# Optimization experiments

Hardware: AMD Instinct MI355X
Metric: run time of the kernel (lower is better)

## Reference

```python
import jax, jax.numpy as jnp
import numpy as np

B, T, V, E, H, M, U, W = 8, 64, 30000, 256, 512, 512, 32, 512


def setup_inputs():
    rng = np.random.RandomState(0)
    ks = jax.random.split(jax.random.key(0), 20)
    u_len = rng.randint(U // 2, U + 1, size=B).astype(np.int32)
    w_len = rng.randint(W // 2, W + 1, size=B).astype(np.int32)
    # word2utt[b, j] = utterance index owning word j; padded words -> last valid utt
    w2u = np.zeros((B, W), np.int32)
    for b in range(B):
        j = np.minimum(np.arange(W), w_len[b] - 1)
        w2u[b] = np.minimum((j * u_len[b]) // w_len[b], u_len[b] - 1)
    s = 0.02
    p = lambda i, shp: jax.random.normal(ks[i], shp, jnp.float32) * s
    emb = p(0, (V, E)).at[0].set(0.0)  # padding_idx=0
    return {
        'target': jax.random.randint(ks[1], (B, T), 0, V, jnp.int32),
        'u_output': jax.random.normal(ks[2], (B, U, M), jnp.float32),
        'w_output': jax.random.normal(ks[3], (B, W, M), jnp.float32),
        'u_len': jnp.asarray(u_len), 'w_len': jnp.asarray(w_len), 'word2utt': jnp.asarray(w2u),
        'emb': emb,
        'W_ih': p(4, (3 * H, E)), 'W_hh': p(5, (3 * H, H)),
        'b_ih': p(6, (3 * H,)), 'b_hh': p(7, (3 * H,)),
        'Wu': p(8, (H, M)), 'bu': p(9, (H,)),
        'Ww': p(10, (H, M)), 'bw': p(11, (H,)),
        'Wo': p(12, (V, H + M)), 'bo': p(13, (V,)),
        'Wd': p(14, (1, V)), 'Wy': p(15, (1, E)),
        'Ws': p(16, (1, H)), 'bs': p(17, (1,)),
    }


def reference(target, u_output, w_output, u_len, w_len, word2utt,
              emb, W_ih, W_hh, b_ih, b_hh, Wu, bu, Ww, bw, Wo, bo, Wd, Wy, Ws, bs):
    Bn = target.shape[0]
    Un = u_output.shape[1]
    Vn = Wo.shape[0]
    Au = jnp.einsum('bum,hm->buh', u_output, Wu) + bu  # attention_u(u_output)
    Aw = jnp.einsum('bwm,hm->bwh', w_output, Ww) + bw  # attention_w(w_output)
    u_mask = jnp.arange(Un)[None, :] < u_len[:, None]               # [B,U]
    w_mask = jnp.arange(w_output.shape[1])[None, :] < w_len[:, None]  # [B,W]
    # initial hidden = last valid utterance state (mem_hidden == dec_hidden)
    h0 = jnp.take_along_axis(u_output, (u_len - 1)[:, None, None], axis=1)[:, 0, :]

    def gru_step(x, h):
        gi = x @ W_ih.T + b_ih
        gh = h @ W_hh.T + b_hh
        ir, iz, inn = jnp.split(gi, 3, axis=-1)
        hr, hz, hn = jnp.split(gh, 3, axis=-1)
        r = jax.nn.sigmoid(ir + hr)
        z = jax.nn.sigmoid(iz + hz)
        n = jnp.tanh(inn + r * hn)
        return (1.0 - z) * n + z * h

    def seg_softmax(sw, seg, valid):  # per-batch ragged per-utterance softmax over words
        swm = jnp.where(valid, sw, -jnp.inf)
        m = jax.ops.segment_max(swm, seg, num_segments=Un)
        e = jnp.where(valid, jnp.exp(sw - m[seg]), 0.0)
        d = jax.ops.segment_sum(e, seg, num_segments=Un)
        return e / d[seg]

    def step(carry, yt):
        h, d_prev, eu_prev = carry
        y = emb[yt]                               # [B,E]
        h_new = gru_step(y, h)                    # rnn_output == new hidden (1 layer)
        su = jnp.einsum('bh,buh->bu', h_new, Au)
        su = jax.nn.softmax(jnp.where(u_mask, su, -jnp.inf), axis=-1)
        gamma = jax.nn.sigmoid(d_prev @ Wd.T + y @ Wy.T + h_new @ Ws.T + bs)  # [B,1]
        su = (1.0 - gamma) * su + gamma * eu_prev
        su = su / jnp.sum(su, axis=-1, keepdims=True)
        sw = jnp.einsum('bh,bwh->bw', h_new, Aw)
        pw = jax.vmap(seg_softmax)(sw, word2utt, w_mask)        # [B,W]
        suw = jnp.take_along_axis(su, word2utt, axis=1) * pw    # [B,W]
        ctx = jnp.einsum('bw,bwm->bm', suw, w_output)
        logits = jnp.concatenate([ctx, h_new], axis=-1) @ Wo.T + bo
        dt = jax.nn.log_softmax(logits, axis=-1)
        return (h_new, dt, su), (dt, suw, su)

    init = (h0, jnp.zeros((Bn, Vn), jnp.float32), jnp.zeros((Bn, Un), jnp.float32))
    _, (dts, suws, sus) = jax.lax.scan(step, init, target.T)
    dec_output = jnp.swapaxes(dts, 0, 1)   # [B,T,V]
    scores_uw = jnp.swapaxes(suws, 0, 1)   # [B,T,W]
    scores_u = jnp.swapaxes(sus, 0, 1)     # [B,T,U]
    return dec_output, scores_uw, scores_u
```

## Files before the change

### kernel.cpp

```cpp
#include <hip/hip_runtime.h>
#include <math.h>

typedef unsigned short ushort_t;
typedef unsigned int uint_t;
typedef unsigned long long ulong_t;
typedef __attribute__((ext_vector_type(8))) short s16x8;
typedef __attribute__((ext_vector_type(4))) float f32x4;

#define BB 8
#define TT 64
#define VV 30000
#define VP 30080
#define EE 256
#define HH 512
#define MM 512
#define UU 32
#define WW 512
#define G3 1536
#define NDB 235
#define NBG 64

#define OFF_GI    0
#define OFF_YALL  786432
#define OFF_WY    917504
#define OFF_H0    918016
#define OFF_HALL  922112
#define OFF_HU    1184256
#define OFF_HW    1446400
#define OFF_HS    1708544
#define OFF_HWV   1709056
#define OFF_P     1709568
#define OFF_SW    1725952
#define OFF_C     1988096
#define OFF_E     6182400
#define OFF_WV    6198784
#define OFF_PART  6200320
#define OFF_LSE   6208512
#define OFF_WOV   6209024
#define OFF_HBT   13909504
#define OFF_SYNC  14040576

#define DEC_SZ (BB*TT*VV)
#define SUW_OFF DEC_SZ
#define SU_OFF  (DEC_SZ + BB*TT*WW)

__device__ __forceinline__ float sigm(float x){ return 1.0f/(1.0f+__expf(-x)); }
__device__ __forceinline__ ushort_t to_bf16(float f){
  uint_t u = __float_as_uint(f);
  return (ushort_t)((u + 0x7fffu + ((u>>16)&1u)) >> 16);
}


template<int TRANSB>
__global__ void __launch_bounds__(256)
k_gemm_b(const float* __restrict__ A, int lda, int aS,
         const float* __restrict__ B, int ldb, int bS,
         const float* __restrict__ bias,
         float* __restrict__ C, int ldc, int cS, int K){
  A += (size_t)blockIdx.z * aS;
  B += (size_t)blockIdx.z * bS;
  C += (size_t)blockIdx.z * cS;
  __shared__ float As[32][65];
  __shared__ float Bs[32][65];
  int tid = threadIdx.x;
  int bx = blockIdx.x, by = blockIdx.y;
  int tx = tid & 15, ty = tid >> 4;
  float acc[4][4] = {};
  for (int k0 = 0; k0 < K; k0 += 32){
    {
      int r = tid >> 2, cbase = (tid & 3) * 8;
      const float* ap = A + (size_t)(by*64 + r)*lda + k0 + cbase;
      #pragma unroll
      for (int i=0;i<8;++i) As[cbase+i][r] = ap[i];
    }
    if (TRANSB){
      int r = tid >> 2, cbase = (tid & 3) * 8;
      const float* bp = B + (size_t)(bx*64 + r)*ldb + k0 + cbase;
      #pragma unroll
      for (int i=0;i<8;++i) Bs[cbase+i][r] = bp[i];
    } else {
      int kk = tid >> 3, cbase = (tid & 7) * 8;
      const float* bp = B + (size_t)(k0 + kk)*ldb + bx*64 + cbase;
      #pragma unroll
      for (int i=0;i<8;++i) Bs[kk][cbase+i] = bp[i];
    }
    __syncthreads();
    #pragma unroll
    for (int kk=0;kk<32;++kk){
      float a0=As[kk][ty*4+0], a1=As[kk][ty*4+1], a2=As[kk][ty*4+2], a3=As[kk][ty*4+3];
      float b0=Bs[kk][tx*4+0], b1=Bs[kk][tx*4+1], b2=Bs[kk][tx*4+2], b3=Bs[kk][tx*4+3];
      acc[0][0]+=a0*b0; acc[0][1]+=a0*b1; acc[0][2]+=a0*b2; acc[0][3]+=a0*b3;
      acc[1][0]+=a1*b0; acc[1][1]+=a1*b1; acc[1][2]+=a1*b2; acc[1][3]+=a1*b3;
      acc[2][0]+=a2*b0; acc[2][1]+=a2*b1; acc[2][2]+=a2*b2; acc[2][3]+=a2*b3;
      acc[3][0]+=a3*b0; acc[3][1]+=a3*b1; acc[3][2]+=a3*b2; acc[3][3]+=a3*b3;
    }
    __syncthreads();
  }
  #pragma unroll
  for (int i=0;i<4;++i){
    int row = by*64 + ty*4 + i;
    #pragma unroll
    for (int j=0;j<4;++j){
      int col = bx*64 + tx*4 + j;
      float v = acc[i][j];
      if (bias) v += bias[col];
      C[(size_t)row*ldc + col] = v;
    }
  }
}

__global__ void k_gather_y(const int* __restrict__ target, const float* __restrict__ emb,
                           float* __restrict__ ws){
  int idx = blockIdx.x*256 + threadIdx.x;
  int bt = idx >> 8; int e = idx & 255;
  int tok = target[bt];
  ws[OFF_YALL + idx] = emb[tok*EE + e];
}

__global__ void k_wy(const float* __restrict__ Wy, float* __restrict__ ws){
  int wid  = blockIdx.x*4 + (threadIdx.x>>6);
  int lane = threadIdx.x & 63;
  const float* y = ws + OFF_YALL + wid*EE;
  float acc = 0.f;
  for (int e=lane; e<EE; e+=64) acc += y[e]*Wy[e];
  for (int off=32; off; off>>=1) acc += __shfl_xor(acc, off);
  if (lane == 0) ws[OFF_WY + wid] = acc;
}

__global__ void k_h0(const float* __restrict__ u_output, const int* __restrict__ u_len,
                     float* __restrict__ ws){
  int idx = blockIdx.x*256 + threadIdx.x;
  int b = idx >> 9; int k = idx & 511;
  int u = u_len[b]-1;
  ws[OFF_H0 + idx] = u_output[(b*UU+u)*MM + k];
}

__global__ void __launch_bounds__(256)
k_wovc(const float* __restrict__ Wo, ushort_t* __restrict__ wov){
  int idx8 = blockIdx.x*256 + threadIdx.x;
  int v = idx8 >> 6;
  int k8 = (idx8 & 63) << 3;
  uint_t u0=0,u1=0,u2=0,u3=0;
  if (v < VV){
    const float* src = Wo + (size_t)v*1024 + k8;
    float4 f0 = *(const float4*)src;
    float4 f1 = *(const float4*)(src+4);
    u0 = (uint_t)to_bf16(f0.x) | ((uint_t)to_bf16(f0.y) << 16);
    u1 = (uint_t)to_bf16(f0.z) | ((uint_t)to_bf16(f0.w) << 16);
    u2 = (uint_t)to_bf16(f1.x) | ((uint_t)to_bf16(f1.y) << 16);
    u3 = (uint_t)to_bf16(f1.z) | ((uint_t)to_bf16(f1.w) << 16);
  }
  uint4 pk = make_uint4(u0,u1,u2,u3);
  *(uint4*)(wov + (size_t)idx8*8) = pk;
}

__global__ void __launch_bounds__(256)
k_wv(const float* __restrict__ Wo, const float* __restrict__ bo,
     const float* __restrict__ Wd, float* __restrict__ wv){
  __shared__ float wds[128];
  __shared__ float red[256];
  int tid = threadIdx.x;
  int v0 = blockIdx.x*128;
  float pbo=0.f, pwd=0.f;
  if (tid < 128){
    int v = v0 + tid;
    float wd = (v<VV)? Wd[v] : 0.f;
    wds[tid] = wd;
    pbo = wd * ((v<VV)? bo[v] : 0.f);
    pwd = wd;
  }
  __syncthreads();
  float4 acc = {0,0,0,0};
  int nmax = (v0 + 128 <= VV) ? 128 : (VV - v0);
  for (int i=0;i<nmax;++i){
    float wd = wds[i];
    float4 w4 = *(const float4*)(Wo + (size_t)(v0+i)*1024 + tid*4);
    acc.x += wd*w4.x; acc.y += wd*w4.y; acc.z += wd*w4.z; acc.w += wd*w4.w;
  }
  atomicAdd(&wv[tid*4+0], acc.x);
  atomicAdd(&wv[tid*4+1], acc.y);
  atomicAdd(&wv[tid*4+2], acc.z);
  atomicAdd(&wv[tid*4+3], acc.w);
  red[tid] = pbo; __syncthreads();
  for (int s=128; s; s>>=1){ if (tid<s) red[tid]+=red[tid+s]; __syncthreads(); }
  if (tid==0) atomicAdd(&wv[1024], red[0]);
  __syncthreads();
  red[tid] = pwd; __syncthreads();
  for (int s=128; s; s>>=1){ if (tid<s) red[tid]+=red[tid+s]; __syncthreads(); }
  if (tid==0) atomicAdd(&wv[1025], red[0]);
}


__global__ void __launch_bounds__(512)
k_gru_persist(const float* __restrict__ W_hh, const float* __restrict__ b_hh,
              float* __restrict__ ws){
  uint_t* flags = (uint_t*)(ws + OFF_SYNC);
  int k    = blockIdx.x*8 + (threadIdx.x>>6);
  int lane = threadIdx.x & 63;
  const float* gi_all = ws + OFF_GI;
  const float* wr = W_hh + (size_t)k*HH;
  const float* wz = W_hh + (size_t)(HH+k)*HH;
  const float* wn = W_hh + (size_t)(2*HH+k)*HH;
  float bhr = b_hh[k], bhz = b_hh[HH+k], bhn = b_hh[2*HH+k];

  for (int t=0; t<TT; ++t){
    const float* hin = (t==0) ? (ws+OFF_H0) : (ws+OFF_HALL + (size_t)(t-1)*4096);
    float* hout = ws + OFF_HALL + (size_t)t*4096;
    float pr[8], pz[8], pn[8];
    #pragma unroll
    for (int b=0;b<8;++b){ pr[b]=0.f; pz[b]=0.f; pn[b]=0.f; }
    #pragma unroll 2
    for (int kk=lane; kk<HH; kk+=64){
      float w1 = wr[kk], w2 = wz[kk], w3 = wn[kk];
      #pragma unroll
      for (int b=0;b<8;++b){
        float hv = hin[b*HH+kk];
        pr[b] += hv*w1; pz[b] += hv*w2; pn[b] += hv*w3;
      }
    }
    #pragma unroll
    for (int off=32; off; off>>=1){
      #pragma unroll
      for (int b=0;b<8;++b){
        pr[b] += __shfl_xor(pr[b],off);
        pz[b] += __shfl_xor(pz[b],off);
        pn[b] += __shfl_xor(pn[b],off);
      }
    }
    if (lane == 0){
      #pragma unroll
      for (int b=0;b<8;++b){
        const float* gi = gi_all + (b*TT + t)*G3;
        float r = sigm(gi[k]      + pr[b] + bhr);
        float z = sigm(gi[HH+k]   + pz[b] + bhz);
        float n = tanhf(gi[2*HH+k] + r*(pn[b] + bhn));
        hout[b*HH+k] = (1.f-z)*n + z*hin[b*HH+k];
      }
    }
    __syncthreads();
    if (threadIdx.x == 0)
      __hip_atomic_store(&flags[blockIdx.x*32], (uint_t)(t+1), __ATOMIC_RELEASE, __HIP_MEMORY_SCOPE_AGENT);
    if ((int)threadIdx.x < NBG){
      while (__hip_atomic_load(&flags[threadIdx.x*32], __ATOMIC_RELAXED, __HIP_MEMORY_SCOPE_AGENT) < (uint_t)(t+1))
        __builtin_amdgcn_s_sleep(1);
    }
    __syncthreads();
  }
  {
    ushort_t* hbt = (ushort_t*)(ws + OFF_HBT);
    int base = (blockIdx.x*512 + threadIdx.x)*8;
    #pragma unroll
    for (int i=0;i<8;++i) hbt[base+i] = to_bf16(ws[OFF_HALL + base + i]);
  }
}


__global__ void __launch_bounds__(256)
k_lh_mfma(const float* __restrict__ Wo, const float* __restrict__ bo,
          const ushort_t* __restrict__ hbt, float* __restrict__ out){
  int tid = threadIdx.x;
  int wv = tid >> 6, l = tid & 63;
  int lm = l & 15, lg = l >> 4;
  int vbase = blockIdx.x*128 + wv*32;
  int rbase = blockIdx.y*128;
  f32x4 acc[2][8];
  #pragma unroll
  for (int s=0;s<2;++s)
    #pragma unroll
    for (int rt=0;rt<8;++rt) acc[s][rt] = (f32x4){0.f,0.f,0.f,0.f};

  for (int k0 = 0; k0 < 512; k0 += 32){
    int kk = k0 + lg*8;
    union { uint_t u[4]; s16x8 s; } af[2];
    #pragma unroll
    for (int s=0;s<2;++s){
      int v = vbase + s*16 + lm; if (v >= VV) v = VV-1;
      const float* ap = Wo + (size_t)v*1024 + 512 + kk;
      float4 f0 = *(const float4*)ap;
      float4 f1 = *(const float4*)(ap+4);
      af[s].u[0] = ((__float_as_uint(f0.x)+0x8000u)>>16) | ((__float_as_uint(f0.y)+0x8000u) & 0xffff0000u);
      af[s].u[1] = ((__float_as_uint(f0.z)+0x8000u)>>16) | ((__float_as_uint(f0.w)+0x8000u) & 0xffff0000u);
      af[s].u[2] = ((__float_as_uint(f1.x)+0x8000u)>>16) | ((__float_as_uint(f1.y)+0x8000u) & 0xffff0000u);
      af[s].u[3] = ((__float_as_uint(f1.z)+0x8000u)>>16) | ((__float_as_uint(f1.w)+0x8000u) & 0xffff0000u);
    }
    #pragma unroll
    for (int rt=0;rt<8;++rt){
      const ushort_t* bp = hbt + (size_t)(rbase + rt*16 + lm)*HH + kk;
      s16x8 bf = *(const s16x8*)bp;
      acc[0][rt] = __builtin_amdgcn_mfma_f32_16x16x32_bf16(af[0].s, bf, acc[0][rt], 0, 0, 0);
      acc[1][rt] = __builtin_amdgcn_mfma_f32_16x16x32_bf16(af[1].s, bf, acc[1][rt], 0, 0, 0);
    }
  }
  float bv[2][4];
  #pragma unroll
  for (int s=0;s<2;++s)
    #pragma unroll
    for (int r=0;r<4;++r){
      int v = vbase + s*16 + lg*4 + r;
      bv[s][r] = (v < VV) ? bo[v] : 0.f;
    }
  #pragma unroll
  for (int rt=0;rt<8;++rt){
    int row = rbase + rt*16 + lm;
    float* orow = out + (size_t)((row&7)*TT + (row>>3))*VV;
    #pragma unroll
    for (int s=0;s<2;++s){
      #pragma unroll
      for (int r=0;r<4;++r){
        int v = vbase + s*16 + lg*4 + r;
        if (v < VV) orow[v] = acc[s][rt][r] + bv[s][r];
      }
    }
  }
}


__global__ void k_hdots(const float* __restrict__ Ws, float* __restrict__ ws){
  int wid  = blockIdx.x*4 + (threadIdx.x>>6);
  int lane = threadIdx.x & 63;
  int row = wid >> 1, which = wid & 1;
  const float* h = ws + OFF_HALL + row*HH;
  const float* src = which ? (ws + OFF_WV + 512) : Ws;
  float acc = 0.f;
  for (int k=lane; k<HH; k+=64) acc += h[k]*src[k];
  for (int off=32; off; off>>=1) acc += __shfl_xor(acc, off);
  if (lane == 0) (which ? ws+OFF_HWV : ws+OFF_HS)[row] = acc;
}

__global__ void k_p(const float* __restrict__ u_output, const int* __restrict__ u_len,
                    float* __restrict__ ws){
  int row = blockIdx.x;
  int b = row & 7;
  int tid = threadIdx.x;
  __shared__ float su_s[UU];
  {
    int u = tid >> 3, l8 = tid & 7;
    const float* hu = ws + OFF_HU + row*512;
    const float* uo = u_output + (size_t)(b*UU + u)*MM;
    float acc = 0.f;
    for (int m=l8; m<MM; m+=8) acc += hu[m]*uo[m];
    acc += __shfl_xor(acc,1); acc += __shfl_xor(acc,2); acc += __shfl_xor(acc,4);
    if (l8 == 0) su_s[u] = acc;
  }
  __syncthreads();
  if (tid < 32){
    int ul = u_len[b];
    float sv = su_s[tid];
    bool valid = tid < ul;
    float mv = valid ? sv : -1e30f;
    for (int off=16; off; off>>=1) mv = fmaxf(mv, __shfl_xor(mv, off));
    float e = valid ? __expf(sv - mv) : 0.f;
    float ssum = e;
    for (int off=16; off; off>>=1) ssum += __shfl_xor(ssum, off);
    ws[OFF_P + row*UU + tid] = e/ssum;
  }
}

__global__ void k_pw(const int* __restrict__ word2utt, const int* __restrict__ w_len,
                     float* __restrict__ ws){
  int row = blockIdx.x;
  int b = row & 7;
  int tid = threadIdx.x;
  __shared__ float sarr[WW];
  __shared__ int   seg[WW];
  __shared__ float marr[UU], darr[UU];
  int wl = w_len[b];
  float* swrow = ws + OFF_SW + row*WW;
  for (int w=tid; w<WW; w+=256){ sarr[w] = swrow[w]; seg[w] = word2utt[b*WW+w]; }
  __syncthreads();
  {
    int g = tid>>3, l8 = tid&7;
    float mv = -1e30f;
    for (int w=l8; w<wl; w+=8) if (seg[w]==g) mv = fmaxf(mv, sarr[w]);
    mv = fmaxf(mv, __shfl_xor(mv,1)); mv = fmaxf(mv, __shfl_xor(mv,2)); mv = fmaxf(mv, __shfl_xor(mv,4));
    float d = 0.f;
    for (int w=l8; w<wl; w+=8) if (seg[w]==g) d += __expf(sarr[w]-mv);
    d += __shfl_xor(d,1); d += __shfl_xor(d,2); d += __shfl_xor(d,4);
    if (l8 == 0){ marr[g]=mv; darr[g]=d; }
  }
  __syncthreads();
  for (int w=tid; w<WW; w+=256){
    float val = 0.f;
    if (w < wl){ int u = seg[w]; val = __expf(sarr[w]-marr[u])/darr[u]; }
    swrow[w] = val;
  }
}

__global__ void __launch_bounds__(256)
k_C(const float* __restrict__ w_output, const int* __restrict__ w_len,
    const int* __restrict__ u_len, const int* __restrict__ word2utt,
    float* __restrict__ ws){
  int row = blockIdx.x;
  int b = row & 7;
  int tid = threadIdx.x;
  __shared__ float pws[WW];
  __shared__ int   seg[WW];
  __shared__ int   st[UU], en[UU];
  __shared__ float wvs[512];
  __shared__ float red4[8];
  int wl = w_len[b], ul = u_len[b];
  const float* pwrow = ws + OFF_SW + row*WW;
  for (int w=tid; w<WW; w+=256){ pws[w] = pwrow[w]; seg[w] = word2utt[b*WW+w]; }
  for (int m=tid; m<512; m+=256) wvs[m] = ws[OFF_WV + m];
  if (tid < UU){ st[tid]=0; en[tid]=0; }
  __syncthreads();
  for (int w=tid; w<wl; w+=256){
    int s = seg[w];
    if (w==0 || seg[w-1]!=s) st[s]=w;
    if (w==wl-1 || seg[w+1]!=s) en[s]=w+1;
  }
  __syncthreads();
  ushort_t* Cu = (ushort_t*)(ws + OFF_C);
  int m0 = tid, m1 = tid + 256;
  int lane = tid & 63, wvi = tid >> 6;
  for (int u=0; u<UU; ++u){
    float acc0=0.f, acc1=0.f;
    if (u < ul){
      int s = st[u], e = en[u];
      for (int w=s; w<e; ++w){
        float p = pws[w];
        const float* wo = w_output + ((size_t)(b*WW+w))*MM;
        acc0 += p*wo[m0];
        acc1 += p*wo[m1];
      }
    }
    size_t cbase = ((size_t)row*UU + u)*512;
    Cu[cbase + m0] = to_bf16(acc0);
    Cu[cbase + m1] = to_bf16(acc1);
    float part = acc0*wvs[m0] + acc1*wvs[m1];
    for (int off=32; off; off>>=1) part += __shfl_xor(part, off);
    if (lane == 0) red4[wvi] = part;
    __syncthreads();
    if (tid == 0) ws[OFF_E + row*UU + u] = red4[0]+red4[1]+red4[2]+red4[3];
    __syncthreads();
  }
}


__global__ void __launch_bounds__(256)
k_decode_persist(const int* __restrict__ u_len, const float* __restrict__ bs,
                 const ushort_t* __restrict__ wov,
                 float* __restrict__ ws, float* __restrict__ out){
  int bid = blockIdx.x;
  int tid = threadIdx.x;
  uint_t* sy     = (uint_t*)(ws + OFF_SYNC);
  uint_t* flags  = sy + 8192;
  uint_t* flags2 = sy + 16000;
  __shared__ float suL[8][32];
  __shared__ float qbufL[8], lseL[8], gamL[8];
  __shared__ int   ulS[8];
  __shared__ uint_t cbU[16*260];
  __shared__ float2 wred[4][8];
  __shared__ float smr[256], ssr[256];
  __shared__ float cst[4];
  if (tid == 0){ cst[0]=bs[0]; cst[1]=ws[OFF_WV+1024]; cst[2]=ws[OFF_WV+1025]; }
  if (tid < 8){ qbufL[tid]=0.f; lseL[tid]=0.f; ulS[tid]=u_len[tid]; }
  suL[tid>>5][tid&31] = 0.f;
  for (int i=tid; i<8*260; i+=256) cbU[8*260 + i] = 0u;
  __syncthreads();

  int wv = tid >> 6, l = tid & 63;
  int lm = l & 15, lgp = l >> 4;

  for (int t=0; t<TT; ++t){
    int b = tid >> 5, j = tid & 31;
    int row = t*8 + b;

    if (t > 0 && tid < 8)
      lseL[tid] = __hip_atomic_load((const float*)(ws + OFF_LSE + (t-1)*8 + tid),
                                    __ATOMIC_RELAXED, __HIP_MEMORY_SCOPE_AGENT);
    __syncthreads();
    if (tid < 8){
      float pd = 0.f;
      if (t > 0)
        pd = qbufL[tid] + ws[OFF_HWV + (t-1)*8 + tid] + cst[1] - lseL[tid]*cst[2];
      gamL[tid] = sigm(pd + ws[OFF_WY + tid*TT + t] + ws[OFF_HS + t*8 + tid] + cst[0]);
    }
    __syncthreads();
    {
      float gg = gamL[b];
      float p = ws[OFF_P + row*UU + j];
      float eu = suL[b][j];
      float mix = (1.f-gg)*p + gg*eu;
      float s2 = mix;
      #pragma unroll
      for (int off=16; off; off>>=1) s2 += __shfl_xor(s2, off);
      float su = mix / s2;
      suL[b][j] = su;
      float qp = su * ws[OFF_E + row*UU + j];
      #pragma unroll
      for (int off=16; off; off>>=1) qp += __shfl_xor(qp, off);
      if (j == 0) qbufL[b] = qp;
    }
    __syncthreads();
    if (bid < 8 && tid < 32)
      out[SU_OFF + (bid*TT + t)*UU + tid] = suL[bid][tid];
    {
      int m16 = j * 16;
      int ul = ulS[b];
      const ushort_t* Crow = (const ushort_t*)(ws + OFF_C) + ((size_t)row*UU)*512 + m16;
      float acc[16];
      #pragma unroll
      for (int i=0;i<16;++i) acc[i]=0.f;
      for (int u=0; u<ul; ++u){
        float su = suL[b][u];
        uint4 c0 = *(const uint4*)(Crow + (size_t)u*512);
        uint4 c1 = *(const uint4*)(Crow + (size_t)u*512 + 8);
        uint_t cc[8] = {c0.x,c0.y,c0.z,c0.w,c1.x,c1.y,c1.z,c1.w};
        #pragma unroll
        for (int q=0;q<8;++q){
          acc[2*q]   += su * __uint_as_float((cc[q] & 0xffffu) << 16);
          acc[2*q+1] += su * __uint_as_float((cc[q] >> 16) << 16);
        }
      }
      #pragma unroll
      for (int q=0;q<8;++q){
        uint_t pk = (uint_t)to_bf16(acc[2*q]) | ((uint_t)to_bf16(acc[2*q+1]) << 16);
        cbU[b*260 + j*8 + q] = pk;
      }
    }
    __syncthreads();

    {
      int v0w = bid*128 + wv*32;
      f32x4 acc0 = {0.f,0.f,0.f,0.f}, acc1 = {0.f,0.f,0.f,0.f};
      const ushort_t* ap0 = wov + (size_t)(v0w + lm)*512 + lgp*8;
      const ushort_t* ap1 = ap0 + 16*512;
      const uint_t* cbrow = cbU + lm*260 + lgp*4;
      #pragma unroll
      for (int ks=0; ks<16; ++ks){
        s16x8 av0 = *(const s16x8*)(ap0 + ks*32);
        s16x8 av1 = *(const s16x8*)(ap1 + ks*32);
        s16x8 bv  = *(const s16x8*)(cbrow + ks*16);
        acc0 = __builtin_amdgcn_mfma_f32_16x16x32_bf16(av0, bv, acc0, 0, 0, 0);
        acc1 = __builtin_amdgcn_mfma_f32_16x16x32_bf16(av1, bv, acc1, 0, 0, 0);
      }
      float pm = -1e30f, ps = 0.f;
      if (lm < 8){
        float* orow = out + ((size_t)(lm*TT + t))*VV;
        float l8v[8];
        #pragma unroll
        for (int vt=0; vt<2; ++vt){
          int vb = v0w + vt*16 + lgp*4;
          f32x4 a = vt ? acc1 : acc0;
          if (vb + 3 < VV){
            float4 o = *(const float4*)(orow + vb);
            float g0 = a[0]+o.x, g1 = a[1]+o.y, g2 = a[2]+o.z, g3 = a[3]+o.w;
            *(float4*)(orow + vb) = make_float4(g0,g1,g2,g3);
            l8v[vt*4+0]=g0; l8v[vt*4+1]=g1; l8v[vt*4+2]=g2; l8v[vt*4+3]=g3;
          } else {
            #pragma unroll
            for (int r=0;r<4;++r){
              int v = vb + r;
              float g = -1e30f;
              if (v < VV){ g = a[r] + orow[v]; orow[v] = g; }
              l8v[vt*4+r] = g;
            }
          }
        }
        #pragma unroll
        for (int i=0;i<8;++i) pm = fmaxf(pm, l8v[i]);
        #pragma unroll
        for (int i=0;i<8;++i) ps += (l8v[i] > -5e29f) ? __expf(l8v[i]-pm) : 0.f;
      }
      #pragma unroll
      for (int off=16; off<=32; off<<=1){
        float mo = __shfl_xor(pm, off);
        float so = __shfl_xor(ps, off);
        float nm = fmaxf(pm, mo);
        ps = ps*__expf(pm-nm) + so*__expf(mo-nm);
        pm = nm;
      }
      if (lgp == 0 && lm < 8) wred[wv][lm] = make_float2(pm, ps);
    }
    __syncthreads();
    if (tid < 8){
      float m = -1e30f, s = 0.f;
      #pragma unroll
      for (int w=0; w<4; ++w){
        float2 e = wred[w][tid];
        float nm = fmaxf(m, e.x);
        s = s*__expf(m-nm) + e.y*__expf(e.x-nm);
        m = nm;
      }
      *(float2*)(ws + OFF_PART + (t&1)*4096 + (bid*8 + tid)*2) = make_float2(m, s);
    }

    __syncthreads();
    if (tid == 0)
      __hip_atomic_store(&flags[bid*32], (uint_t)(t+1), __ATOMIC_RELEASE, __HIP_MEMORY_SCOPE_AGENT);
    if (bid < 8){
      if (tid < NDB){
        while (__hip_atomic_load(&flags[tid*32], __ATOMIC_RELAXED, __HIP_MEMORY_SCOPE_AGENT) < (uint_t)(t+1))
          __builtin_amdgcn_s_sleep(2);
      }
      __syncthreads();
      {
        const ulong_t* partq = (const ulong_t*)(ws + OFF_PART + (t&1)*4096);
        float m = -1e30f, s = 0.f;
        if (tid < NDB){
          ulong_t pq = __hip_atomic_load(&partq[tid*8 + bid], __ATOMIC_RELAXED, __HIP_MEMORY_SCOPE_AGENT);
          m = __uint_as_float((uint_t)pq);
          s = __uint_as_float((uint_t)(pq >> 32));
        }
        smr[tid]=m; ssr[tid]=s; __syncthreads();
        for (int st=128; st; st>>=1){
          if (tid < st){
            float m1 = smr[tid], s1 = ssr[tid];
            float m2 = smr[tid+st], s2 = ssr[tid+st];
            float mm = fmaxf(m1, m2);
            ssr[tid] = s1*__expf(m1-mm) + s2*__expf(m2-mm);
            smr[tid] = mm;
          }
          __syncthreads();
        }
        if (tid == 0){
          __hip_atomic_store((float*)(ws + OFF_LSE + t*8 + bid), smr[0] + logf(ssr[0]),
                             __ATOMIC_RELAXED, __HIP_MEMORY_SCOPE_AGENT);
          __hip_atomic_store(&flags2[bid*32], (uint_t)(t+1), __ATOMIC_RELEASE, __HIP_MEMORY_SCOPE_AGENT);
        }
      }
    }
    if (tid < 8){
      while (__hip_atomic_load(&flags2[tid*32], __ATOMIC_RELAXED, __HIP_MEMORY_SCOPE_AGENT) < (uint_t)(t+1))
        __builtin_amdgcn_s_sleep(1);
    }
    __syncthreads();
  }
}


__global__ void k_sub2(const float* __restrict__ ws, float* __restrict__ out){
  int v = blockIdx.x*256 + threadIdx.x;
  int tb = blockIdx.y;
  int t = tb >> 3, b = tb & 7;
  if (v < VV) out[(size_t)(b*TT+t)*VV + v] -= ws[OFF_LSE + tb];
}

__global__ void k_suw2(const int* __restrict__ word2utt, const float* __restrict__ ws,
                       float* __restrict__ out){
  int row = blockIdx.x;
  int t = row >> 3, b = row & 7;
  int tid = threadIdx.x;
  for (int w=tid; w<WW; w+=256){
    int seg = word2utt[b*WW + w];
    float su = out[SU_OFF + (b*TT+t)*UU + seg];
    float pw = ws[OFF_SW + row*WW + w];
    out[SUW_OFF + (b*TT+t)*WW + w] = su*pw;
  }
}

extern "C" void kernel_launch(void* const* d_in, const int* in_sizes, int n_in,
                              void* d_out, int out_size, void* d_ws, size_t ws_size,
                              hipStream_t stream) {
  const int*   target   = (const int*)d_in[0];
  const float* u_output = (const float*)d_in[1];
  const float* w_output = (const float*)d_in[2];
  const int*   u_len    = (const int*)d_in[3];
  const int*   w_len    = (const int*)d_in[4];
  const int*   word2utt = (const int*)d_in[5];
  const float* emb      = (const float*)d_in[6];
  const float* W_ih     = (const float*)d_in[7];
  const float* W_hh     = (const float*)d_in[8];
  const float* b_ih     = (const float*)d_in[9];
  const float* b_hh     = (const float*)d_in[10];
  const float* Wu       = (const float*)d_in[11];
  const float* Ww       = (const float*)d_in[13];
  const float* Wo       = (const float*)d_in[15];
  const float* bo       = (const float*)d_in[16];
  const float* Wd       = (const float*)d_in[17];
  const float* Wy       = (const float*)d_in[18];
  const float* Ws       = (const float*)d_in[19];
  const float* bs       = (const float*)d_in[20];
  float* out = (float*)d_out;
  float* ws  = (float*)d_ws;
  ushort_t* wov = (ushort_t*)(ws + OFF_WOV);
  ushort_t* hbt = (ushort_t*)(ws + OFF_HBT);

  hipMemsetAsync(ws + OFF_SYNC, 0, 16384*sizeof(float), stream);

  hipLaunchKernelGGL(k_gather_y, dim3(512), dim3(256), 0, stream, target, emb, ws);
  hipLaunchKernelGGL((k_gemm_b<1>), dim3(24,8,1), dim3(256), 0, stream,
                     ws+OFF_YALL, 256, 0, W_ih, 256, 0, b_ih, ws+OFF_GI, 1536, 0, 256);
  hipLaunchKernelGGL(k_wy, dim3(128), dim3(256), 0, stream, Wy, ws);
  hipLaunchKernelGGL(k_h0, dim3(16), dim3(256), 0, stream, u_output, u_len, ws);
  hipLaunchKernelGGL(k_wovc, dim3(7520), dim3(256), 0, stream, Wo, wov);
  hipMemsetAsync(ws + OFF_WV, 0, 1536*sizeof(float), stream);
  hipLaunchKernelGGL(k_wv, dim3(235), dim3(256), 0, stream, Wo, bo, Wd, ws+OFF_WV);

  hipLaunchKernelGGL(k_gru_persist, dim3(NBG), dim3(512), 0, stream, W_hh, b_hh, ws);

  hipLaunchKernelGGL(k_lh_mfma, dim3(235, 4), dim3(256), 0, stream, Wo, bo, hbt, out);
  hipLaunchKernelGGL((k_gemm_b<0>), dim3(8,8,1), dim3(256), 0, stream,
                     ws+OFF_HALL, 512, 0, Wu, 512, 0, (const float*)nullptr, ws+OFF_HU, 512, 0, 512);
  hipLaunchKernelGGL((k_gemm_b<0>), dim3(8,8,1), dim3(256), 0, stream,
                     ws+OFF_HALL, 512, 0, Ww, 512, 0, (const float*)nullptr, ws+OFF_HW, 512, 0, 512);
  hipLaunchKernelGGL(k_hdots, dim3(256), dim3(256), 0, stream, Ws, ws);
  hipLaunchKernelGGL(k_p, dim3(512), dim3(256), 0, stream, u_output, u_len, ws);
  hipLaunchKernelGGL((k_gemm_b<1>), dim3(8,1,8), dim3(256), 0, stream,
                     ws+OFF_HW, 4096, 512, w_output, 512, 262144, (const float*)nullptr,
                     ws+OFF_SW, 4096, 512, 512);
  hipLaunchKernelGGL(k_pw, dim3(512), dim3(256), 0, stream, word2utt, w_len, ws);
  hipLaunchKernelGGL(k_C, dim3(512), dim3(256), 0, stream,
                     w_output, w_len, u_len, word2utt, ws);

  hipLaunchKernelGGL(k_decode_persist, dim3(NDB), dim3(256), 0, stream,
                     u_len, bs, wov, ws, out);

  hipLaunchKernelGGL(k_sub2, dim3(118, 512), dim3(256), 0, stream, ws, out);
  hipLaunchKernelGGL(k_suw2, dim3(512), dim3(256), 0, stream, word2utt, ws, out);
}
```

Before: 2.072 ms.

## Double threads in GRU and decode persistent kernels, fuse embedding gather with Wy dot

```diff
diff --git a/kernel.cpp b/kernel.cpp
--- a/kernel.cpp
+++ b/kernel.cpp
@@ -109,22 +109,18 @@
   }
 }
 
-__global__ void k_gather_y(const int* __restrict__ target, const float* __restrict__ emb,
-                           float* __restrict__ ws){
-  int idx = blockIdx.x*256 + threadIdx.x;
-  int bt = idx >> 8; int e = idx & 255;
+__global__ void k_y(const int* __restrict__ target, const float* __restrict__ emb,
+                    const float* __restrict__ Wy, float* __restrict__ ws){
+  int bt = blockIdx.x;
+  int e = threadIdx.x;
+  __shared__ float r[256];
   int tok = target[bt];
-  ws[OFF_YALL + idx] = emb[tok*EE + e];
-}
-
-__global__ void k_wy(const float* __restrict__ Wy, float* __restrict__ ws){
-  int wid  = blockIdx.x*4 + (threadIdx.x>>6);
-  int lane = threadIdx.x & 63;
-  const float* y = ws + OFF_YALL + wid*EE;
-  float acc = 0.f;
-  for (int e=lane; e<EE; e+=64) acc += y[e]*Wy[e];
-  for (int off=32; off; off>>=1) acc += __shfl_xor(acc, off);
-  if (lane == 0) ws[OFF_WY + wid] = acc;
+  float v = emb[tok*EE + e];
+  ws[OFF_YALL + bt*EE + e] = v;
+  r[e] = v * Wy[e];
+  __syncthreads();
+  for (int s=128; s; s>>=1){ if (e<s) r[e]+=r[e+s]; __syncthreads(); }
+  if (e == 0) ws[OFF_WY + bt] = r[0];
 }
 
 __global__ void k_h0(const float* __restrict__ u_output, const int* __restrict__ u_len,
@@ -191,17 +187,21 @@
 }
 
 
-__global__ void __launch_bounds__(512)
+__global__ void __launch_bounds__(1024)
 k_gru_persist(const float* __restrict__ W_hh, const float* __restrict__ b_hh,
               float* __restrict__ ws){
   uint_t* flags = (uint_t*)(ws + OFF_SYNC);
-  int k    = blockIdx.x*8 + (threadIdx.x>>6);
-  int lane = threadIdx.x & 63;
+  int tid  = threadIdx.x;
+  int wid  = tid >> 6;
+  int lane = tid & 63;
+  int half = wid >> 3;
+  int kl   = wid & 7;
+  int k    = blockIdx.x*8 + kl;
   const float* gi_all = ws + OFF_GI;
   const float* wr = W_hh + (size_t)k*HH;
   const float* wz = W_hh + (size_t)(HH+k)*HH;
   const float* wn = W_hh + (size_t)(2*HH+k)*HH;
-  float bhr = b_hh[k], bhz = b_hh[HH+k], bhn = b_hh[2*HH+k];
+  __shared__ float red[16][24];
 
   for (int t=0; t<TT; ++t){
     const float* hin = (t==0) ? (ws+OFF_H0) : (ws+OFF_HALL + (size_t)(t-1)*4096);
@@ -209,8 +209,10 @@
     float pr[8], pz[8], pn[8];
     #pragma unroll
     for (int b=0;b<8;++b){ pr[b]=0.f; pz[b]=0.f; pn[b]=0.f; }
-    #pragma unroll 2
-    for (int kk=lane; kk<HH; kk+=64){
+    int kk0 = half*256 + lane;
+    #pragma unroll
+    for (int it=0; it<4; ++it){
+      int kk = kk0 + it*64;
       float w1 = wr[kk], w2 = wz[kk], w3 = wn[kk];
       #pragma unroll
       for (int b=0;b<8;++b){
@@ -230,27 +232,38 @@
     if (lane == 0){
       #pragma unroll
       for (int b=0;b<8;++b){
-        const float* gi = gi_all + (b*TT + t)*G3;
-        float r = sigm(gi[k]      + pr[b] + bhr);
-        float z = sigm(gi[HH+k]   + pz[b] + bhz);
-        float n = tanhf(gi[2*HH+k] + r*(pn[b] + bhn));
-        hout[b*HH+k] = (1.f-z)*n + z*hin[b*HH+k];
-      }
-    }
-    __syncthreads();
-    if (threadIdx.x == 0)
+        red[wid][b]    = pr[b];
+        red[wid][8+b]  = pz[b];
+        red[wid][16+b] = pn[b];
+      }
+    }
+    __syncthreads();
+    if (tid < 64){
+      int klx = tid >> 3, b = tid & 7;
+      int k2 = blockIdx.x*8 + klx;
+      float prs = red[klx][b]    + red[8+klx][b];
+      float pzs = red[klx][8+b]  + red[8+klx][8+b];
+      float pns = red[klx][16+b] + red[8+klx][16+b];
+      const float* gi = gi_all + (b*TT + t)*G3;
+      float r = sigm(gi[k2]      + prs + b_hh[k2]);
+      float z = sigm(gi[HH+k2]   + pzs + b_hh[HH+k2]);
+      float n = tanhf(gi[2*HH+k2] + r*(pns + b_hh[2*HH+k2]));
+      hout[b*HH+k2] = (1.f-z)*n + z*hin[b*HH+k2];
+    }
+    __syncthreads();
+    if (tid == 0)
       __hip_atomic_store(&flags[blockIdx.x*32], (uint_t)(t+1), __ATOMIC_RELEASE, __HIP_MEMORY_SCOPE_AGENT);
-    if ((int)threadIdx.x < NBG){
-      while (__hip_atomic_load(&flags[threadIdx.x*32], __ATOMIC_RELAXED, __HIP_MEMORY_SCOPE_AGENT) < (uint_t)(t+1))
+    if (tid < NBG){
+      while (__hip_atomic_load(&flags[tid*32], __ATOMIC_RELAXED, __HIP_MEMORY_SCOPE_AGENT) < (uint_t)(t+1))
         __builtin_amdgcn_s_sleep(1);
     }
     __syncthreads();
   }
   {
     ushort_t* hbt = (ushort_t*)(ws + OFF_HBT);
-    int base = (blockIdx.x*512 + threadIdx.x)*8;
-    #pragma unroll
-    for (int i=0;i<8;++i) hbt[base+i] = to_bf16(ws[OFF_HALL + base + i]);
+    int base = (blockIdx.x*1024 + tid)*4;
+    #pragma unroll
+    for (int i=0;i<4;++i) hbt[base+i] = to_bf16(ws[OFF_HALL + base + i]);
   }
 }
 
@@ -397,7 +410,7 @@
   __shared__ int   seg[WW];
   __shared__ int   st[UU], en[UU];
   __shared__ float wvs[512];
-  __shared__ float red4[8];
+  __shared__ float red32[UU][4];
   int wl = w_len[b], ul = u_len[b];
   const float* pwrow = ws + OFF_SW + row*WW;
   for (int w=tid; w<WW; w+=256){ pws[w] = pwrow[w]; seg[w] = word2utt[b*WW+w]; }
@@ -428,16 +441,17 @@
     Cu[cbase + m0] = to_bf16(acc0);
     Cu[cbase + m1] = to_bf16(acc1);
     float part = acc0*wvs[m0] + acc1*wvs[m1];
+    #pragma unroll
     for (int off=32; off; off>>=1) part += __shfl_xor(part, off);
-    if (lane == 0) red4[wvi] = part;
-    __syncthreads();
-    if (tid == 0) ws[OFF_E + row*UU + u] = red4[0]+red4[1]+red4[2]+red4[3];
-    __syncthreads();
-  }
-}
-
-
-__global__ void __launch_bounds__(256)
+    if (lane == 0) red32[u][wvi] = part;
+  }
+  __syncthreads();
+  if (tid < UU)
+    ws[OFF_E + row*UU + tid] = red32[tid][0]+red32[tid][1]+red32[tid][2]+red32[tid][3];
+}
+
+
+__global__ void __launch_bounds__(512)
 k_decode_persist(const int* __restrict__ u_len, const float* __restrict__ bs,
                  const ushort_t* __restrict__ wov,
                  float* __restrict__ ws, float* __restrict__ out){
@@ -450,22 +464,19 @@
   __shared__ float qbufL[8], lseL[8], gamL[8];
   __shared__ int   ulS[8];
   __shared__ uint_t cbU[16*260];
-  __shared__ float2 wred[4][8];
+  __shared__ float2 wred[8][8];
   __shared__ float smr[256], ssr[256];
   __shared__ float cst[4];
   if (tid == 0){ cst[0]=bs[0]; cst[1]=ws[OFF_WV+1024]; cst[2]=ws[OFF_WV+1025]; }
   if (tid < 8){ qbufL[tid]=0.f; lseL[tid]=0.f; ulS[tid]=u_len[tid]; }
-  suL[tid>>5][tid&31] = 0.f;
-  for (int i=tid; i<8*260; i+=256) cbU[8*260 + i] = 0u;
-  __syncthreads();
-
-  int wv = tid >> 6, l = tid & 63;
+  if (tid < 256) suL[tid>>5][tid&31] = 0.f;
+  for (int i=tid; i<8*260; i+=512) cbU[8*260 + i] = 0u;
+  __syncthreads();
+
+  int wid = tid >> 6, l = tid & 63;
   int lm = l & 15, lgp = l >> 4;
 
   for (int t=0; t<TT; ++t){
-    int b = tid >> 5, j = tid & 31;
-    int row = t*8 + b;
-
     if (t > 0 && tid < 8)
       lseL[tid] = __hip_atomic_load((const float*)(ws + OFF_LSE + (t-1)*8 + tid),
                                     __ATOMIC_RELAXED, __HIP_MEMORY_SCOPE_AGENT);
@@ -477,7 +488,9 @@
       gamL[tid] = sigm(pd + ws[OFF_WY + tid*TT + t] + ws[OFF_HS + t*8 + tid] + cst[0]);
     }
     __syncthreads();
-    {
+    if (tid < 256){
+      int b = tid >> 5, j = tid & 31;
+      int row = t*8 + b;
       float gg = gamL[b];
       float p = ws[OFF_P + row*UU + j];
       float eu = suL[b][j];
@@ -496,72 +509,66 @@
     if (bid < 8 && tid < 32)
       out[SU_OFF + (bid*TT + t)*UU + tid] = suL[bid][tid];
     {
-      int m16 = j * 16;
+      int b = tid >> 6, l64 = tid & 63;
+      int m8 = l64 * 8;
+      int row = t*8 + b;
       int ul = ulS[b];
-      const ushort_t* Crow = (const ushort_t*)(ws + OFF_C) + ((size_t)row*UU)*512 + m16;
-      float acc[16];
-      #pragma unroll
-      for (int i=0;i<16;++i) acc[i]=0.f;
+      const ushort_t* Crow = (const ushort_t*)(ws + OFF_C) + ((size_t)row*UU)*512 + m8;
+      float acc[8];
+      #pragma unroll
+      for (int i=0;i<8;++i) acc[i]=0.f;
       for (int u=0; u<ul; ++u){
         float su = suL[b][u];
         uint4 c0 = *(const uint4*)(Crow + (size_t)u*512);
-        uint4 c1 = *(const uint4*)(Crow + (size_t)u*512 + 8);
-        uint_t cc[8] = {c0.x,c0.y,c0.z,c0.w,c1.x,c1.y,c1.z,c1.w};
+        uint_t cc[4] = {c0.x,c0.y,c0.z,c0.w};
         #pragma unroll
-        for (int q=0;q<8;++q){
+        for (int q=0;q<4;++q){
           acc[2*q]   += su * __uint_as_float((cc[q] & 0xffffu) << 16);
           acc[2*q+1] += su * __uint_as_float((cc[q] >> 16) << 16);
         }
       }
       #pragma unroll
-      for (int q=0;q<8;++q){
+      for (int q=0;q<4;++q){
         uint_t pk = (uint_t)to_bf16(acc[2*q]) | ((uint_t)to_bf16(acc[2*q+1]) << 16);
-        cbU[b*260 + j*8 + q] = pk;
+        cbU[b*260 + l64*4 + q] = pk;
       }
     }
     __syncthreads();
 
     {
-      int v0w = bid*128 + wv*32;
-      f32x4 acc0 = {0.f,0.f,0.f,0.f}, acc1 = {0.f,0.f,0.f,0.f};
-      const ushort_t* ap0 = wov + (size_t)(v0w + lm)*512 + lgp*8;
-      const ushort_t* ap1 = ap0 + 16*512;
+      int vbase = bid*128 + wid*16;
+      f32x4 acc0 = {0.f,0.f,0.f,0.f};
+      const ushort_t* ap0 = wov + (size_t)(vbase + lm)*512 + lgp*8;
       const uint_t* cbrow = cbU + lm*260 + lgp*4;
       #pragma unroll
       for (int ks=0; ks<16; ++ks){
         s16x8 av0 = *(const s16x8*)(ap0 + ks*32);
-        s16x8 av1 = *(const s16x8*)(ap1 + ks*32);
         s16x8 bv  = *(const s16x8*)(cbrow + ks*16);
         acc0 = __builtin_amdgcn_mfma_f32_16x16x32_bf16(av0, bv, acc0, 0, 0, 0);
-        acc1 = __builtin_amdgcn_mfma_f32_16x16x32_bf16(av1, bv, acc1, 0, 0, 0);
       }
       float pm = -1e30f, ps = 0.f;
       if (lm < 8){
         float* orow = out + ((size_t)(lm*TT + t))*VV;
-        float l8v[8];
-        #pragma unroll
-        for (int vt=0; vt<2; ++vt){
-          int vb = v0w + vt*16 + lgp*4;
-          f32x4 a = vt ? acc1 : acc0;
-          if (vb + 3 < VV){
-            float4 o = *(const float4*)(orow + vb);
-            float g0 = a[0]+o.x, g1 = a[1]+o.y, g2 = a[2]+o.z, g3 = a[3]+o.w;
-            *(float4*)(orow + vb) = make_float4(g0,g1,g2,g3);
-            l8v[vt*4+0]=g0; l8v[vt*4+1]=g1; l8v[vt*4+2]=g2; l8v[vt*4+3]=g3;
-          } else {
-            #pragma unroll
-            for (int r=0;r<4;++r){
-              int v = vb + r;
-              float g = -1e30f;
-              if (v < VV){ g = a[r] + orow[v]; orow[v] = g; }
-              l8v[vt*4+r] = g;
-            }
+        int vb = vbase + lgp*4;
+        float l4v[4];
+        if (vb + 3 < VV){
+          float4 o = *(const float4*)(orow + vb);
+          float g0 = acc0[0]+o.x, g1 = acc0[1]+o.y, g2 = acc0[2]+o.z, g3 = acc0[3]+o.w;
+          *(float4*)(orow + vb) = make_float4(g0,g1,g2,g3);
+          l4v[0]=g0; l4v[1]=g1; l4v[2]=g2; l4v[3]=g3;
+        } else {
+          #pragma unroll
+          for (int r=0;r<4;++r){
+            int v = vb + r;
+            float g = -1e30f;
+            if (v < VV){ g = acc0[r] + orow[v]; orow[v] = g; }
+            l4v[r] = g;
           }
         }
         #pragma unroll
-        for (int i=0;i<8;++i) pm = fmaxf(pm, l8v[i]);
+        for (int i=0;i<4;++i) pm = fmaxf(pm, l4v[i]);
         #pragma unroll
-        for (int i=0;i<8;++i) ps += (l8v[i] > -5e29f) ? __expf(l8v[i]-pm) : 0.f;
+        for (int i=0;i<4;++i) ps += (l4v[i] > -5e29f) ? __expf(l4v[i]-pm) : 0.f;
       }
       #pragma unroll
       for (int off=16; off<=32; off<<=1){
@@ -571,13 +578,13 @@
         ps = ps*__expf(pm-nm) + so*__expf(mo-nm);
         pm = nm;
       }
-      if (lgp == 0 && lm < 8) wred[wv][lm] = make_float2(pm, ps);
+      if (lgp == 0 && lm < 8) wred[wid][lm] = make_float2(pm, ps);
     }
     __syncthreads();
     if (tid < 8){
       float m = -1e30f, s = 0.f;
       #pragma unroll
-      for (int w=0; w<4; ++w){
+      for (int w=0; w<8; ++w){
         float2 e = wred[w][tid];
         float nm = fmaxf(m, e.x);
         s = s*__expf(m-nm) + e.y*__expf(e.x-nm);
@@ -603,7 +610,8 @@
           m = __uint_as_float((uint_t)pq);
           s = __uint_as_float((uint_t)(pq >> 32));
         }
-        smr[tid]=m; ssr[tid]=s; __syncthreads();
+        if (tid < 256){ smr[tid]=m; ssr[tid]=s; }
+        __syncthreads();
         for (int st=128; st; st>>=1){
           if (tid < st){
             float m1 = smr[tid], s1 = ssr[tid];
@@ -679,16 +687,15 @@
 
   hipMemsetAsync(ws + OFF_SYNC, 0, 16384*sizeof(float), stream);
 
-  hipLaunchKernelGGL(k_gather_y, dim3(512), dim3(256), 0, stream, target, emb, ws);
+  hipLaunchKernelGGL(k_y, dim3(512), dim3(256), 0, stream, target, emb, Wy, ws);
   hipLaunchKernelGGL((k_gemm_b<1>), dim3(24,8,1), dim3(256), 0, stream,
                      ws+OFF_YALL, 256, 0, W_ih, 256, 0, b_ih, ws+OFF_GI, 1536, 0, 256);
-  hipLaunchKernelGGL(k_wy, dim3(128), dim3(256), 0, stream, Wy, ws);
   hipLaunchKernelGGL(k_h0, dim3(16), dim3(256), 0, stream, u_output, u_len, ws);
   hipLaunchKernelGGL(k_wovc, dim3(7520), dim3(256), 0, stream, Wo, wov);
   hipMemsetAsync(ws + OFF_WV, 0, 1536*sizeof(float), stream);
   hipLaunchKernelGGL(k_wv, dim3(235), dim3(256), 0, stream, Wo, bo, Wd, ws+OFF_WV);
 
-  hipLaunchKernelGGL(k_gru_persist, dim3(NBG), dim3(512), 0, stream, W_hh, b_hh, ws);
+  hipLaunchKernelGGL(k_gru_persist, dim3(NBG), dim3(1024), 0, stream, W_hh, b_hh, ws);
 
   hipLaunchKernelGGL(k_lh_mfma, dim3(235, 4), dim3(256), 0, stream, Wo, bo, hbt, out);
   hipLaunchKernelGGL((k_gemm_b<0>), dim3(8,8,1), dim3(256), 0, stream,
@@ -704,7 +711,7 @@
   hipLaunchKernelGGL(k_C, dim3(512), dim3(256), 0, stream,
                      w_output, w_len, u_len, word2utt, ws);
 
-  hipLaunchKernelGGL(k_decode_persist, dim3(NDB), dim3(256), 0, stream,
+  hipLaunchKernelGGL(k_decode_persist, dim3(NDB), dim3(512), 0, stream,
                      u_len, bs, wov, ws, out);
 
   hipLaunchKernelGGL(k_sub2, dim3(118, 512), dim3(256), 0, stream, ws, out);
```

Result: faster. 1.929 ms (-6.9%).
